# Performance work log

Hardware: AMD Instinct MI355X
Metric: run time of the kernel (lower is better)

## Reference

```python
import jax, jax.numpy as jnp
import numpy as np

B, DIM, HEADS, WS, H, W = 8, 192, 6, 8, 128, 128
HD = DIM // HEADS


def _make_coords(h, w, ws):
    # matches torch buffers: channel 0 = x (width axis), channel 1 = y (height axis)
    ref_w = jnp.linspace(-1.0, 1.0, w)
    ref_h = jnp.linspace(-1.0, 1.0, h)
    img_ref = jnp.stack(jnp.meshgrid(ref_w, ref_h, indexing='ij'), 0).transpose(0, 2, 1)  # (2,h,w)
    wh, ww = h // ws, w // ws
    win_ref = img_ref.reshape(2, wh, ws, ww, ws).mean(axis=(2, 4)).reshape(2, wh, 1, ww, 1)
    bch = jnp.arange(ws) * 2.0 / (h - 1); bch = bch - bch.mean()
    bcw = jnp.arange(ws) * 2.0 / (w - 1); bcw = bcw - bcw.mean()
    ech = jnp.tile(bch, wh)                      # (wh*ws,)
    ecw = jnp.tile(bcw, ww)                      # (ww*ws,)
    offs = jnp.stack(jnp.meshgrid(ecw, ech, indexing='ij'), 0).transpose(0, 2, 1)  # (2, wh*ws, ww*ws)
    offs = offs.reshape(2, wh, ws, ww, ws)
    return win_ref + offs, offs


def _rel_index(ws):
    ch, cw = np.meshgrid(np.arange(ws), np.arange(ws), indexing='ij')
    cf = np.stack([ch.ravel(), cw.ravel()])           # (2, ws*ws)
    rel = cf[:, :, None] - cf[:, None, :]             # (2, n, n)
    return jnp.asarray((rel[0] + ws - 1) * (2 * ws - 1) + (rel[1] + ws - 1))


def _grid_sample(img, grid):
    # F.grid_sample: bilinear, padding_mode='zeros', align_corners=True
    # img (N,C,H,W), grid (N,Ho,Wo,2) with [..,0]=x, [..,1]=y in [-1,1]
    n, c, h, w = img.shape
    gx = (grid[..., 0] + 1.0) * 0.5 * (w - 1)
    gy = (grid[..., 1] + 1.0) * 0.5 * (h - 1)
    x0 = jnp.floor(gx); y0 = jnp.floor(gy)
    wx1 = gx - x0; wy1 = gy - y0

    def gather(ix, iy, wgt):
        valid = (ix >= 0) & (ix <= w - 1) & (iy >= 0) & (iy <= h - 1)
        ixc = jnp.clip(ix, 0, w - 1).astype(jnp.int32)
        iyc = jnp.clip(iy, 0, h - 1).astype(jnp.int32)
        vals = jax.vmap(lambda im, yy, xx: im[:, yy, xx])(img, iyc, ixc)  # (N,C,Ho,Wo)
        return vals * (wgt * valid)[:, None]

    return (gather(x0, y0, (1 - wx1) * (1 - wy1)) + gather(x0 + 1, y0, wx1 * (1 - wy1))
            + gather(x0, y0 + 1, (1 - wx1) * wy1) + gather(x0 + 1, y0 + 1, wx1 * wy1))


def _forward(x, var, qkv_w, qkv_b, bias_w, bias_b, scale_w, scale_b, proj_w, proj_b, rel_table):
    b, c, h, w = x.shape
    wh, ww = h // WS, w // WS
    n_pred = b * HEADS
    base, offs = _make_coords(h, w, WS)

    topk = int(0.8 * h * w)
    var3 = var.reshape(b, c, h * w)
    _, idx = jax.lax.top_k(var3, topk)
    bi = jnp.arange(b)[:, None, None]; ci = jnp.arange(c)[None, :, None]
    mask = jnp.zeros((b, c, h * w), bool).at[bi, ci, idx].set(True)
    x_var = x * jnp.where(mask, 1.0, 0.6).reshape(b, c, h, w).astype(x.dtype)

    # sampling biases/scales: AvgPool(ws) -> LeakyReLU -> 1x1 conv
    pooled = jax.nn.leaky_relu(x_var.reshape(b, c, wh, WS, ww, WS).mean(axis=(3, 5)))
    biases = (jnp.einsum('bchw,oc->bohw', pooled, bias_w) + bias_b[None, :, None, None])
    biases = biases.reshape(n_pred, 2, wh, ww) / jnp.array([w // WS, h // WS], x.dtype)[None, :, None, None]
    scales = (jnp.einsum('bchw,oc->bohw', pooled, scale_w) + scale_b[None, :, None, None]).reshape(n_pred, 2, wh, ww)

    coords = base[None] + offs[None] * scales[:, :, :, None, :, None] + biases[:, :, :, None, :, None]
    grid = coords.transpose(0, 2, 3, 4, 5, 1).reshape(n_pred, h, w, 2)

    # qkv 1x1 conv, split into per-head maps
    qkv = jnp.einsum('bchw,oc->bohw', x, qkv_w) + qkv_b[None, :, None, None]
    qkv = qkv.reshape(b, 3, HEADS, HD, h, w).transpose(1, 0, 2, 3, 4, 5).reshape(3, n_pred, HD, h, w)
    q, k, v = qkv[0], qkv[1], qkv[2]

    ks = _grid_sample(k, grid)
    vs = _grid_sample(v, grid)

    def to_windows(t):  # (b*heads, hd, h, w) -> (b*wh*ww, heads, ws*ws, hd)
        return t.reshape(b, HEADS, HD, wh, WS, ww, WS).transpose(0, 3, 5, 1, 4, 6, 2).reshape(b * wh * ww, HEADS, WS * WS, HD)

    qw, kw, vw = to_windows(q), to_windows(ks), to_windows(vs)
    scores = jnp.einsum('wnid,wnjd->wnij', qw, kw) * (HD ** -0.5)
    rel_bias = rel_table[_rel_index(WS)].transpose(2, 0, 1)  # (heads, ws*ws, ws*ws)
    attn = jax.nn.softmax(scores + rel_bias[None], axis=-1)
    out = jnp.einsum('wnij,wnjd->wnid', attn, vw)
    out = out.reshape(b, wh, ww, HEADS, WS, WS, HD).transpose(0, 3, 6, 1, 4, 2, 5).reshape(b, c, h, w)
    return jnp.einsum('bchw,oc->bohw', out, proj_w) + proj_b[None, :, None, None]


def setup_inputs() -> dict:
    key = jax.random.key(0)
    ks = jax.random.split(key, 8)
    f = jnp.float32
    return {
        'x': jax.random.normal(ks[0], (B, DIM, H, W), f),
        'var': jax.random.uniform(ks[1], (B, DIM, H, W), f),
        'qkv_w': jax.random.normal(ks[2], (3 * DIM, DIM), f) * 0.05,
        'qkv_b': jnp.zeros((3 * DIM,), f),
        'bias_w': jax.random.normal(ks[3], (2 * HEADS, DIM), f) * 0.05,
        'bias_b': jnp.zeros((2 * HEADS,), f),
        'scale_w': jax.random.normal(ks[4], (2 * HEADS, DIM), f) * 0.05,
        'scale_b': jnp.zeros((2 * HEADS,), f),
        'proj_w': jax.random.normal(ks[5], (DIM, DIM), f) * 0.05,
        'proj_b': jnp.zeros((DIM,), f),
        'rel_table': jax.random.normal(ks[6], ((2 * WS - 1) ** 2, HEADS), f) * 0.02,
    }


def reference(x, var, qkv_w, qkv_b, bias_w, bias_b, scale_w, scale_b, proj_w, proj_b, rel_table):
    return _forward(x, var, qkv_w, qkv_b, bias_w, bias_b, scale_w, scale_b, proj_w, proj_b, rel_table)
```

## Files before the change

### kernel.cpp

```cpp
#include <hip/hip_runtime.h>
#include <hip/hip_bf16.h>
#include <math.h>

constexpr int BB = 8, CCH = 192, IH = 128, IW = 128;
constexpr int WSZ = 8;
constexpr int NWIN = 256;
constexpr int NH = 6, HDIM = 32;
constexpr int NPIX = IH * IW;
constexpr int TOPK = 13107;

typedef __attribute__((ext_vector_type(8))) short bf16x8;
typedef __attribute__((ext_vector_type(4))) float f32x4;
typedef __attribute__((ext_vector_type(4))) unsigned short u16x4;
typedef __attribute__((ext_vector_type(8))) unsigned short u16x8;

__device__ __forceinline__ unsigned short f2bf(float f) {
    __hip_bfloat16 h = __float2bfloat16(f);
    return __builtin_bit_cast(unsigned short, h);
}
__device__ __forceinline__ float bf2f(unsigned short u) {
    return __uint_as_float((unsigned)u << 16);
}
__device__ __forceinline__ unsigned monot(float f) {
    unsigned u = __float_as_uint(f);
    return (u & 0x80000000u) ? ~u : (u | 0x80000000u);
}

struct K1Smem {
    unsigned histP[2][2048];
    unsigned hist256[256];
    unsigned wtot[8];
    unsigned s_prefix, s_rem, s_cnt, s_thr, s_need;
    unsigned candKey[320], candIdx[320];
    unsigned cand_cnt, eq_cnt;
    unsigned eq_idx[64];
    float pooled_s[256];
};
struct K0Smem {
    unsigned short T[64][200];
};
constexpr size_t MEGA1_SMEM = sizeof(K0Smem) > sizeof(K1Smem) ? sizeof(K0Smem) : sizeof(K1Smem);

__global__ __launch_bounds__(512) void mega1(const float* __restrict__ x,
                                             const float* __restrict__ var,
                                             float* __restrict__ pooled,
                                             unsigned short* __restrict__ xt,
                                             const float* __restrict__ qkv_w,
                                             const float* __restrict__ proj_w,
                                             unsigned short* __restrict__ wbf,
                                             int fast) {
    __shared__ __align__(16) char smem[MEGA1_SMEM];
    int id = blockIdx.x;
    int tid = threadIdx.x;
    int wv = tid >> 6, lane = tid & 63;

    if (id < 72) {
        int i4 = id * 512 + tid;
        float4 v = (i4 < 27648) ? ((const float4*)qkv_w)[i4]
                                : ((const float4*)proj_w)[i4 - 27648];
        u16x4 pk = { f2bf(v.x), f2bf(v.y), f2bf(v.z), f2bf(v.w) };
        ((u16x4*)wbf)[i4] = pk;
        return;
    }
    id -= 72;

    int role, sub;
    if (fast) {
        int g = id / 7, r = id % 7;
        if (r < 3) { role = 0; sub = 3 * g + r; }
        else       { role = 1; sub = 4 * g + (r - 3); }
    } else {
        role = 0; sub = id;
    }

    if (role == 1) {
        K0Smem& S0 = *(K0Smem*)smem;
        int b = sub >> 8, px0 = (sub & 255) * 64;
        int px = tid & 63, cg = tid >> 6;
#pragma unroll
        for (int j8 = 0; j8 < 3; ++j8) {
            u16x8 pk;
#pragma unroll
            for (int j = 0; j < 8; ++j)
                pk[j] = f2bf(x[(size_t)(b * CCH + cg * 24 + j8 * 8 + j) * NPIX + px0 + px]);
            *(u16x8*)&S0.T[px][cg * 24 + j8 * 8] = pk;
        }
        __syncthreads();
#pragma unroll
        for (int i = 0; i < 3; ++i) {
            int u = tid + 512 * i;
            int p2 = u / 24, cb = u % 24;
            *(u16x8*)&xt[((size_t)(b * NPIX) + px0 + p2) * CCH + cb * 8] = *(const u16x8*)&S0.T[p2][cb * 8];
        }
        return;
    }

    K1Smem& S = *(K1Smem*)smem;
    int row = sub;
    const float4* vrow4 = (const float4*)(var + (size_t)row * NPIX);
    const float4* xrow4 = (const float4*)(x + (size_t)row * NPIX);
    const float* xrow = x + (size_t)row * NPIX;
    constexpr int CAP = 320;

    for (int i = tid; i < 2 * 2048; i += 512) ((unsigned*)S.histP)[i] = 0;
    if (tid < 256) S.pooled_s[tid] = 0.f;
    if (tid == 0) { S.cand_cnt = 0; S.eq_cnt = 0; }
    __syncthreads();

    int hc = lane & 1;
#pragma unroll
    for (int j = 0; j < 8; ++j) {
        float4 v4 = vrow4[tid + 512 * j];
        float vv[4] = {v4.x, v4.y, v4.z, v4.w};
#pragma unroll
        for (int c = 0; c < 4; ++c) {
            unsigned bk = monot(vv[c]) >> 20;
            atomicAdd(&S.histP[hc][bk >> 1], 1u << ((bk & 1) << 4));
        }
    }
    __syncthreads();

    {
        unsigned h8[8]; unsigned tsum = 0;
#pragma unroll
        for (int w = 0; w < 4; ++w) {
            unsigned w0 = S.histP[0][tid * 4 + w];
            unsigned w1 = S.histP[1][tid * 4 + w];
            h8[2 * w]     = (w0 & 0xFFFFu) + (w1 & 0xFFFFu);
            h8[2 * w + 1] = (w0 >> 16) + (w1 >> 16);
            tsum += h8[2 * w] + h8[2 * w + 1];
        }
        unsigned s = tsum;
#pragma unroll
        for (int off = 1; off < 64; off <<= 1) {
            unsigned t = __shfl(s, lane + off);
            if (lane + off < 64) s += t;
        }
        if (lane == 0) S.wtot[wv] = s;
        __syncthreads();
        unsigned crossTot = 0;
        for (int w = wv + 1; w < 8; ++w) crossTot += S.wtot[w];
        unsigned above = crossTot + (s - tsum);
        if (above < TOPK && above + tsum >= TOPK) {
            unsigned cum = above;
            for (int i = 7; i >= 0; --i) {
                if (cum < TOPK && cum + h8[i] >= TOPK) {
                    S.s_prefix = (unsigned)(tid * 8 + i);
                    S.s_rem = TOPK - cum;
                    S.s_cnt = h8[i];
                }
                cum += h8[i];
            }
        }
    }
    __syncthreads();

    unsigned prefix = S.s_prefix, rem2 = S.s_rem, cnt = S.s_cnt;
    int prefbits = 12;

    while (cnt > CAP && prefbits < 32) {
        int nb = (32 - prefbits >= 8) ? 8 : (32 - prefbits);
        int nbuck = 1 << nb;
        __syncthreads();
        for (int i = tid; i < nbuck; i += 512) S.hist256[i] = 0;
        __syncthreads();
        int shift = 32 - prefbits - nb;
#pragma unroll
        for (int j = 0; j < 8; ++j) {
            float4 v4 = vrow4[tid + 512 * j];
            float vv[4] = {v4.x, v4.y, v4.z, v4.w};
#pragma unroll
            for (int c = 0; c < 4; ++c) {
                unsigned mm = monot(vv[c]);
                if ((mm >> (nb + shift)) == prefix)
                    atomicAdd(&S.hist256[(mm >> shift) & (nbuck - 1)], 1u);
            }
        }
        __syncthreads();
        if (wv == 0) {
            int bpl = nbuck > 64 ? nbuck / 64 : 1;
            int nlanes = nbuck / bpl;
            unsigned hh[4] = {0, 0, 0, 0};
            unsigned lsum = 0;
#pragma unroll
            for (int i = 0; i < 4; ++i) {
                if (i < bpl && lane < nlanes) hh[i] = S.hist256[lane * bpl + i];
                lsum += hh[i];
            }
            unsigned s = lsum;
#pragma unroll
            for (int off = 1; off < 64; off <<= 1) {
                unsigned t = __shfl(s, lane + off);
                if (lane + off < 64) s += t;
            }
            unsigned above = s - lsum;
            if (lane < nlanes && above < rem2 && above + lsum >= rem2) {
                unsigned cum = above;
                for (int i = bpl - 1; i >= 0; --i) {
                    if (cum < rem2 && cum + hh[i] >= rem2) {
                        S.s_prefix = (prefix << nb) | (unsigned)(lane * bpl + i);
                        S.s_rem = rem2 - cum;
                        S.s_cnt = hh[i];
                    }
                    cum += hh[i];
                }
            }
        }
        __syncthreads();
        prefix = S.s_prefix; rem2 = S.s_rem; cnt = S.s_cnt;
        prefbits += nb;
    }

    int pshift = 32 - prefbits;

#pragma unroll
    for (int j = 0; j < 8; ++j) {
        float4 v4 = vrow4[tid + 512 * j];
        float4 x4 = xrow4[tid + 512 * j];
        float vv[4] = {v4.x, v4.y, v4.z, v4.w};
        float xv[4] = {x4.x, x4.y, x4.z, x4.w};
        float part = 0.f;
#pragma unroll
        for (int c = 0; c < 4; ++c) {
            unsigned mm = monot(vv[c]);
            unsigned g = (pshift == 0) ? mm : (mm >> pshift);
            float mult = (g > prefix) ? 1.0f : 0.6f;
            if (g == prefix) {
                unsigned pos = atomicAdd(&S.cand_cnt, 1u);
                if (pos < CAP) {
                    S.candKey[pos] = mm;
                    S.candIdx[pos] = (unsigned)(4 * tid + 2048 * j + c);
                }
            }
            part += xv[c] * mult;
        }
        part += __shfl_xor(part, 1);
        part += __shfl_xor(part, 32);
        if ((lane & 1) == 0 && lane < 32)
            atomicAdd(&S.pooled_s[(2 * j + (tid >> 8)) * 16 + ((tid >> 1) & 15)], part);
    }
    __syncthreads();

    int cc = (int)min(S.cand_cnt, (unsigned)CAP);
    for (int ci = tid; ci < cc; ci += 512) {
        unsigned my = S.candKey[ci];
        unsigned kgt = 0, keq = 0;
        for (int e = 0; e < cc; ++e) {
            unsigned o = S.candKey[e];
            kgt += (o > my);
            keq += (o == my);
        }
        if (kgt < rem2 && kgt + keq >= rem2) {
            S.s_thr = my;
            S.s_need = rem2 - kgt;
        }
    }
    __syncthreads();
    unsigned thr = S.s_thr, need_eq = S.s_need;
    for (int ci = tid; ci < cc; ci += 512)
        if (S.candKey[ci] == thr) {
            unsigned pos = atomicAdd(&S.eq_cnt, 1u);
            if (pos < 64) S.eq_idx[pos] = S.candIdx[ci];
        }
    __syncthreads();
    int ecnt = (int)min(S.eq_cnt, 64u);
    if (tid == 0) {
        for (int a = 1; a < ecnt; ++a) {
            unsigned key = S.eq_idx[a]; int q = a - 1;
            while (q >= 0 && S.eq_idx[q] > key) { S.eq_idx[q + 1] = S.eq_idx[q]; --q; }
            S.eq_idx[q + 1] = key;
        }
    }
    __syncthreads();

    for (int ci = tid; ci < cc; ci += 512) {
        unsigned key = S.candKey[ci], idx = S.candIdx[ci];
        bool inset;
        if (key > thr) inset = true;
        else if (key < thr) inset = false;
        else {
            unsigned rank = 0;
            for (int e = 0; e < ecnt; ++e) rank += (S.eq_idx[e] < idx);
            inset = (rank < need_eq);
        }
        if (inset) {
            int y = (int)(idx >> 7), xx = (int)(idx & 127);
            atomicAdd(&S.pooled_s[(y >> 3) * 16 + (xx >> 3)], 0.4f * xrow[idx]);
        }
    }
    __syncthreads();

    if (tid < 256) {
        float s = S.pooled_s[tid] * (1.0f / 64.0f);
        float pv = s > 0.f ? s : 0.01f * s;
        pooled[(size_t)row * NWIN + tid] = pv;
    }
}

template <bool FAST>
__global__ __launch_bounds__(256) void mega2(const float* __restrict__ x,
                                             const unsigned short* __restrict__ xt,
                                             const unsigned short* __restrict__ wq,
                                             const float* __restrict__ qkv_b,
                                             unsigned short* __restrict__ qb,
                                             unsigned short* __restrict__ kb,
                                             unsigned short* __restrict__ vb,
                                             const float* __restrict__ pooled,
                                             const float* __restrict__ bias_w,
                                             const float* __restrict__ bias_b,
                                             const float* __restrict__ scale_w,
                                             const float* __restrict__ scale_b,
                                             float* __restrict__ sb) {
    constexpr int BN = 128, KC = 64, KCP = 72;
    __shared__ unsigned short Ws[CCH][KCP];
    __shared__ unsigned short Xt[BN][KCP];
    int id = blockIdx.x;
    int tid = threadIdx.x;
    int g = id / 7, r = id % 7;

    if (r == 0) {
        float* pcol = (float*)&Ws[0][0];
        float* res = pcol + 4 * CCH;
        int wv = tid >> 6, lane = tid & 63;
        int blk = g * 4 + wv;
        int b = blk >> 8, w = blk & 255;
        for (int c = lane; c < CCH; c += 64) pcol[wv * CCH + c] = pooled[(size_t)(b * CCH + c) * NWIN + w];
        __syncthreads();
        if (lane < 24) {
            bool isScale = lane >= 12;
            int o = isScale ? lane - 12 : lane;
            const float* Wt = isScale ? scale_w : bias_w;
            float acc = 0.f;
            for (int c = 0; c < CCH; ++c) acc += Wt[o * CCH + c] * pcol[wv * CCH + c];
            acc += (isScale ? scale_b[o] : bias_b[o]);
            if (!isScale) acc *= (1.0f / 16.0f);
            res[wv * 24 + lane] = acc;
        }
        __syncthreads();
        if (lane < NH) {
            int p = b * NH + lane;
            float4 v;
            v.x = res[wv * 24 + 12 + 2 * lane];
            v.y = res[wv * 24 + 12 + 2 * lane + 1];
            v.z = res[wv * 24 + 2 * lane];
            v.w = res[wv * 24 + 2 * lane + 1];
            ((float4*)sb)[(size_t)p * NWIN + w] = v;
        }
        return;
    }

    int k3id = 6 * g + (r - 1);
    int px0 = (k3id & 127) * BN;
    int t = (k3id >> 7) % 3;
    int b = k3id / 384;
    int o0 = t * CCH;
    int wv = tid >> 6, lane = tid & 63, lr = lane & 15, lg = lane >> 4;

    f32x4 acc[3][8];
#pragma unroll
    for (int i = 0; i < 3; ++i)
#pragma unroll
        for (int j = 0; j < 8; ++j) acc[i][j] = (f32x4){0.f, 0.f, 0.f, 0.f};

    int spx = tid & 127, skg = tid >> 7;

    for (int k0 = 0; k0 < CCH; k0 += KC) {
#pragma unroll
        for (int i = 0; i < 6; ++i) {
            int u = tid + 256 * i;
            int o = u >> 3, kb8 = u & 7;
            *(u16x8*)&Ws[o][kb8 * 8] = *(const u16x8*)&wq[(size_t)(o0 + o) * CCH + k0 + kb8 * 8];
        }
        if (FAST) {
#pragma unroll
            for (int i = 0; i < 4; ++i) {
                int u = tid + 256 * i;
                int px = u >> 3, kb8 = u & 7;
                *(u16x8*)&Xt[px][kb8 * 8] =
                    *(const u16x8*)&xt[((size_t)(b * NPIX) + px0 + px) * CCH + k0 + kb8 * 8];
            }
        } else {
            const float* xcol = &x[(size_t)(b * CCH + k0 + skg * 32) * NPIX + px0 + spx];
#pragma unroll
            for (int j8 = 0; j8 < 4; ++j8) {
                u16x8 pk;
#pragma unroll
                for (int j = 0; j < 8; ++j) pk[j] = f2bf(xcol[(size_t)(j8 * 8 + j) * NPIX]);
                *(u16x8*)&Xt[spx][skg * 32 + j8 * 8] = pk;
            }
        }
        __syncthreads();
#pragma unroll
        for (int kk = 0; kk < KC; kk += 32) {
            bf16x8 af[3], bfr[8];
#pragma unroll
            for (int i = 0; i < 3; ++i)
                af[i] = *(const bf16x8*)&Ws[wv * 48 + i * 16 + lr][kk + lg * 8];
#pragma unroll
            for (int j = 0; j < 8; ++j)
                bfr[j] = *(const bf16x8*)&Xt[j * 16 + lr][kk + lg * 8];
#pragma unroll
            for (int i = 0; i < 3; ++i)
#pragma unroll
                for (int j = 0; j < 8; ++j)
                    acc[i][j] = __builtin_amdgcn_mfma_f32_16x16x32_bf16(af[i], bfr[j], acc[i][j], 0, 0, 0);
        }
        __syncthreads();
    }

#pragma unroll
    for (int i = 0; i < 3; ++i) {
        int och = wv * 48 + i * 16 + lg * 4;
        float b0 = qkv_b[o0 + och], b1 = qkv_b[o0 + och + 1];
        float b2 = qkv_b[o0 + och + 2], b3 = qkv_b[o0 + och + 3];
#pragma unroll
        for (int j = 0; j < 8; ++j) {
            int px = px0 + lr + j * 16;
            u16x4 pk = { f2bf(acc[i][j][0] + b0), f2bf(acc[i][j][1] + b1),
                         f2bf(acc[i][j][2] + b2), f2bf(acc[i][j][3] + b3) };
            if (t == 0) {
                *(u16x4*)&qb[((size_t)b * NPIX + px) * CCH + och] = pk;
            } else {
                int head = och >> 5, d = och & 31;
                unsigned short* dst = (t == 1) ? kb : vb;
                *(u16x4*)&dst[(((size_t)(b * NH + head)) * NPIX + px) * HDIM + d] = pk;
            }
        }
    }
}

__global__ __launch_bounds__(256) void k4_attn(unsigned short* __restrict__ qatt,
                                               const unsigned short* __restrict__ kb,
                                               const unsigned short* __restrict__ vb,
                                               const float* __restrict__ sb,
                                               const float* __restrict__ rel_table) {
    int tid = threadIdx.x;
    int wv = tid >> 6, lane = tid & 63, lr = lane & 15, lg = lane >> 4;
    int head = blockIdx.y, b = blockIdx.z;
    int win = blockIdx.x * 4 + wv;
    int wy = win >> 4, wx = win & 15;
    int p = b * NH + head;

    __shared__ float rel_s[225];
    __shared__ unsigned short Vl[4][64][33];
    __shared__ unsigned short Pl[4][64][68];

    if (tid < 225) rel_s[tid] = rel_table[tid * NH + head];

    bf16x8 qf[4];
#pragma unroll
    for (int tq = 0; tq < 4; ++tq) {
        int q = tq * 16 + lr;
        int pix = (wy * 8 + (q >> 3)) * IW + wx * 8 + (q & 7);
        qf[tq] = *(const bf16x8*)&qatt[((size_t)b * NPIX + pix) * CCH + head * HDIM + lg * 8];
    }

    float4 sbv = ((const float4*)sb)[(size_t)p * NWIN + win];
    bf16x8 kf[4];
#pragma unroll
    for (int mi = 0; mi < 4; ++mi) {
        int px = mi * 16 + lr;
        int dy = px >> 3, dx = px & 7;
        int yg = wy * 8 + dy, xg = wx * 8 + dx;
        float gx = -1.0f + xg * (2.0f / 127.0f) + ((float)dx - 3.5f) * (2.0f / 127.0f) * sbv.x + sbv.z;
        float gy = -1.0f + yg * (2.0f / 127.0f) + ((float)dy - 3.5f) * (2.0f / 127.0f) * sbv.y + sbv.w;
        float fx = (gx + 1.0f) * 0.5f * 127.0f;
        float fy = (gy + 1.0f) * 0.5f * 127.0f;
        float x0f = floorf(fx), y0f = floorf(fy);
        float wx1 = fx - x0f, wy1 = fy - y0f;
        int ix0 = (int)x0f, iy0 = (int)y0f;
        int ix1 = ix0 + 1, iy1 = iy0 + 1;
        float w00 = (1.0f - wx1) * (1.0f - wy1);
        float w10 = wx1 * (1.0f - wy1);
        float w01 = (1.0f - wx1) * wy1;
        float w11 = wx1 * wy1;
        bool vX0 = (ix0 >= 0) && (ix0 < IW), vX1 = (ix1 >= 0) && (ix1 < IW);
        bool vY0 = (iy0 >= 0) && (iy0 < IH), vY1 = (iy1 >= 0) && (iy1 < IH);
        if (!(vX0 && vY0)) w00 = 0.f;
        if (!(vX1 && vY0)) w10 = 0.f;
        if (!(vX0 && vY1)) w01 = 0.f;
        if (!(vX1 && vY1)) w11 = 0.f;
        int cx0 = min(max(ix0, 0), IW - 1), cx1 = min(max(ix1, 0), IW - 1);
        int cy0 = min(max(iy0, 0), IH - 1), cy1 = min(max(iy1, 0), IH - 1);
        size_t r00 = ((size_t)p * NPIX + cy0 * IW + cx0) * HDIM + lg * 8;
        size_t r10 = ((size_t)p * NPIX + cy0 * IW + cx1) * HDIM + lg * 8;
        size_t r01 = ((size_t)p * NPIX + cy1 * IW + cx0) * HDIM + lg * 8;
        size_t r11 = ((size_t)p * NPIX + cy1 * IW + cx1) * HDIM + lg * 8;
        u16x8 k00 = *(const u16x8*)&kb[r00], k10 = *(const u16x8*)&kb[r10];
        u16x8 k01 = *(const u16x8*)&kb[r01], k11 = *(const u16x8*)&kb[r11];
        u16x8 v00 = *(const u16x8*)&vb[r00], v10 = *(const u16x8*)&vb[r10];
        u16x8 v01 = *(const u16x8*)&vb[r01], v11 = *(const u16x8*)&vb[r11];
#pragma unroll
        for (int c = 0; c < 8; ++c) {
            float kvv = w00 * bf2f(k00[c]) + w10 * bf2f(k10[c]) +
                        w01 * bf2f(k01[c]) + w11 * bf2f(k11[c]);
            float vvv = w00 * bf2f(v00[c]) + w10 * bf2f(v10[c]) +
                        w01 * bf2f(v01[c]) + w11 * bf2f(v11[c]);
            kf[mi][c] = (short)f2bf(kvv);
            Vl[wv][px][lg * 8 + c] = f2bf(vvv);
        }
    }

    f32x4 acc[4][4];
#pragma unroll
    for (int tk = 0; tk < 4; ++tk)
#pragma unroll
        for (int tq = 0; tq < 4; ++tq) acc[tk][tq] = (f32x4){0.f, 0.f, 0.f, 0.f};
#pragma unroll
    for (int tk = 0; tk < 4; ++tk)
#pragma unroll
        for (int tq = 0; tq < 4; ++tq)
            acc[tk][tq] = __builtin_amdgcn_mfma_f32_16x16x32_bf16(kf[tk], qf[tq], acc[tk][tq], 0, 0, 0);

    __syncthreads();

    const float scale = 0.17677669529663688f;
    int qh[4], qwv[4];
#pragma unroll
    for (int tq = 0; tq < 4; ++tq) { int q = tq * 16 + lr; qh[tq] = q >> 3; qwv[tq] = q & 7; }
    float mx[4] = {-1e30f, -1e30f, -1e30f, -1e30f};
#pragma unroll
    for (int tk = 0; tk < 4; ++tk)
#pragma unroll
        for (int r = 0; r < 4; ++r) {
            int key = tk * 16 + lg * 4 + r;
            int kh = key >> 3, kw = key & 7;
#pragma unroll
            for (int tq = 0; tq < 4; ++tq) {
                float v = acc[tk][tq][r] * scale + rel_s[(qh[tq] - kh + 7) * 15 + (qwv[tq] - kw + 7)];
                acc[tk][tq][r] = v;
                mx[tq] = fmaxf(mx[tq], v);
            }
        }
#pragma unroll
    for (int tq = 0; tq < 4; ++tq) {
        mx[tq] = fmaxf(mx[tq], __shfl_xor(mx[tq], 16));
        mx[tq] = fmaxf(mx[tq], __shfl_xor(mx[tq], 32));
    }
    float sm[4] = {0.f, 0.f, 0.f, 0.f};
#pragma unroll
    for (int tk = 0; tk < 4; ++tk)
#pragma unroll
        for (int tq = 0; tq < 4; ++tq)
#pragma unroll
            for (int r = 0; r < 4; ++r) {
                float e = __expf(acc[tk][tq][r] - mx[tq]);
                acc[tk][tq][r] = e;
                sm[tq] += e;
            }
    float inv[4];
#pragma unroll
    for (int tq = 0; tq < 4; ++tq) {
        float s = sm[tq];
        s += __shfl_xor(s, 16);
        s += __shfl_xor(s, 32);
        inv[tq] = 1.0f / s;
    }
#pragma unroll
    for (int tq = 0; tq < 4; ++tq)
#pragma unroll
        for (int tk = 0; tk < 4; ++tk) {
            u16x4 pk = { f2bf(acc[tk][tq][0] * inv[tq]), f2bf(acc[tk][tq][1] * inv[tq]),
                         f2bf(acc[tk][tq][2] * inv[tq]), f2bf(acc[tk][tq][3] * inv[tq]) };
            *(u16x4*)&Pl[wv][tq * 16 + lr][tk * 16 + lg * 4] = pk;
        }

    __syncthreads();

    f32x4 o[4][2];
#pragma unroll
    for (int mq = 0; mq < 4; ++mq)
#pragma unroll
        for (int nd = 0; nd < 2; ++nd) o[mq][nd] = (f32x4){0.f, 0.f, 0.f, 0.f};
#pragma unroll
    for (int ks = 0; ks < 2; ++ks) {
        bf16x8 Af[4];
#pragma unroll
        for (int mq = 0; mq < 4; ++mq) {
            u16x4 lo = *(const u16x4*)&Pl[wv][mq * 16 + lr][ks * 32 + lg * 8];
            u16x4 hi = *(const u16x4*)&Pl[wv][mq * 16 + lr][ks * 32 + lg * 8 + 4];
#pragma unroll
            for (int c = 0; c < 4; ++c) { Af[mq][c] = (short)lo[c]; Af[mq][c + 4] = (short)hi[c]; }
        }
        bf16x8 Bf[2];
#pragma unroll
        for (int nd = 0; nd < 2; ++nd)
#pragma unroll
            for (int j = 0; j < 8; ++j)
                Bf[nd][j] = (short)Vl[wv][ks * 32 + lg * 8 + j][nd * 16 + lr];
#pragma unroll
        for (int mq = 0; mq < 4; ++mq)
#pragma unroll
            for (int nd = 0; nd < 2; ++nd)
                o[mq][nd] = __builtin_amdgcn_mfma_f32_16x16x32_bf16(Af[mq], Bf[nd], o[mq][nd], 0, 0, 0);
    }

#pragma unroll
    for (int mq = 0; mq < 4; ++mq)
#pragma unroll
        for (int nd = 0; nd < 2; ++nd)
#pragma unroll
            for (int r = 0; r < 4; ++r) {
                int q = mq * 16 + lg * 4 + r;
                int pix = (wy * 8 + (q >> 3)) * IW + wx * 8 + (q & 7);
                qatt[((size_t)b * NPIX + pix) * CCH + head * HDIM + nd * 16 + lr] = f2bf(o[mq][nd][r]);
            }
}

__global__ __launch_bounds__(256) void k5_mfma(const unsigned short* __restrict__ att,
                                               const unsigned short* __restrict__ wp,
                                               const float* __restrict__ proj_b,
                                               float* __restrict__ out) {
    constexpr int BN = 128, KC = 64, KCP = 72;
    __shared__ unsigned short Ws[CCH][KCP];
    __shared__ unsigned short Xt[BN][KCP];
    int px0 = blockIdx.x * BN;
    int b = blockIdx.y;
    int tid = threadIdx.x;
    int wv = tid >> 6, lane = tid & 63, lr = lane & 15, lg = lane >> 4;

    f32x4 acc[3][8];
#pragma unroll
    for (int i = 0; i < 3; ++i)
#pragma unroll
        for (int j = 0; j < 8; ++j) acc[i][j] = (f32x4){0.f, 0.f, 0.f, 0.f};

    int spx = tid & 127, skg = tid >> 7;

    for (int k0 = 0; k0 < CCH; k0 += KC) {
#pragma unroll
        for (int i = 0; i < 6; ++i) {
            int u = tid + 256 * i;
            int o = u >> 3, kb8 = u & 7;
            *(u16x8*)&Ws[o][kb8 * 8] = *(const u16x8*)&wp[(size_t)o * CCH + k0 + kb8 * 8];
        }
        {
            const unsigned short* arow = &att[((size_t)b * NPIX + px0 + spx) * CCH + k0 + skg * 32];
#pragma unroll
            for (int j8 = 0; j8 < 4; ++j8)
                *(u16x8*)&Xt[spx][skg * 32 + j8 * 8] = *(const u16x8*)&arow[j8 * 8];
        }
        __syncthreads();
#pragma unroll
        for (int kk = 0; kk < KC; kk += 32) {
            bf16x8 af[3], bfr[8];
#pragma unroll
            for (int i = 0; i < 3; ++i)
                af[i] = *(const bf16x8*)&Ws[wv * 48 + i * 16 + lr][kk + lg * 8];
#pragma unroll
            for (int j = 0; j < 8; ++j)
                bfr[j] = *(const bf16x8*)&Xt[j * 16 + lr][kk + lg * 8];
#pragma unroll
            for (int i = 0; i < 3; ++i)
#pragma unroll
                for (int j = 0; j < 8; ++j)
                    acc[i][j] = __builtin_amdgcn_mfma_f32_16x16x32_bf16(af[i], bfr[j], acc[i][j], 0, 0, 0);
        }
        __syncthreads();
    }

#pragma unroll
    for (int i = 0; i < 3; ++i) {
        int och = wv * 48 + i * 16 + lg * 4;
#pragma unroll
        for (int r = 0; r < 4; ++r) {
            float bias = proj_b[och + r];
            size_t base = (size_t)(b * CCH + och + r) * NPIX + px0 + lr;
#pragma unroll
            for (int j = 0; j < 8; ++j)
                out[base + j * 16] = acc[i][j][r] + bias;
        }
    }
}

extern "C" void kernel_launch(void* const* d_in, const int* in_sizes, int n_in,
                              void* d_out, int out_size, void* d_ws, size_t ws_size,
                              hipStream_t stream) {
    const float* x = (const float*)d_in[0];
    const float* var = (const float*)d_in[1];
    const float* qkv_w = (const float*)d_in[2];
    const float* qkv_b = (const float*)d_in[3];
    const float* bias_w = (const float*)d_in[4];
    const float* bias_b = (const float*)d_in[5];
    const float* scale_w = (const float*)d_in[6];
    const float* scale_b = (const float*)d_in[7];
    const float* proj_w = (const float*)d_in[8];
    const float* proj_b = (const float*)d_in[9];
    const float* rel_table = (const float*)d_in[10];
    float* out = (float*)d_out;

    char* ws = (char*)d_ws;
    float* pooled = (float*)ws;
    float* sb = (float*)(ws + 1572864ull);
    const size_t elemQ = (size_t)BB * CCH * NPIX;
    unsigned short* q = (unsigned short*)(ws + 1769472ull);
    unsigned short* k = q + elemQ;
    unsigned short* v = k + elemQ;
    unsigned short* wbf = v + elemQ;
    unsigned short* wq_bf = wbf;
    unsigned short* wp_bf = wbf + 110592;
    unsigned short* xt = wbf + 147456;

    size_t need_base = 1769472ull + 3ull * elemQ * 2 + 294912ull;
    size_t need_fast = need_base + elemQ * 2;
    if (ws_size < need_base) return;
    bool fast = ws_size >= need_fast;

    mega1<<<dim3(72 + (fast ? 3584 : 1536)), dim3(512), 0, stream>>>(
        x, var, pooled, xt, qkv_w, proj_w, wbf, fast ? 1 : 0);

    if (fast) {
        mega2<true><<<dim3(3584), dim3(256), 0, stream>>>(x, xt, wq_bf, qkv_b, q, k, v,
                                                          pooled, bias_w, bias_b, scale_w, scale_b, sb);
    } else {
        mega2<false><<<dim3(3584), dim3(256), 0, stream>>>(x, xt, wq_bf, qkv_b, q, k, v,
                                                           pooled, bias_w, bias_b, scale_w, scale_b, sb);
    }

    k4_attn<<<dim3(NWIN / 4, NH, BB), dim3(256), 0, stream>>>(q, k, v, sb, rel_table);
    k5_mfma<<<dim3(NPIX / 128, BB), dim3(256), 0, stream>>>(q, wp_bf, proj_b, out);
}
```

Before: 267.1 us.

## Pass softmax probabilities to PV MFMA via lane shuffles instead of LDS

In the windowed attention kernel, the probability matrix is no longer staged through a shared-memory buffer (Pl). Each MFMA A-operand for the P·V product is built from the QK accumulators with cross-lane shuffles, which removes one LDS round trip and one block-wide barrier. The barrier moves to before the QK MFMAs, and s_setprio hints are placed around the MFMA sequences. In exchange it issues many ds_bpermute shuffles (two per element plus a select), which may cost as much as the LDS traffic they replace.

```diff
diff --git a/kernel.cpp b/kernel.cpp
--- a/kernel.cpp
+++ b/kernel.cpp
@@ -443,7 +443,6 @@
 
     __shared__ float rel_s[225];
     __shared__ unsigned short Vl[4][64][33];
-    __shared__ unsigned short Pl[4][64][68];
 
     if (tid < 225) rel_s[tid] = rel_table[tid * NH + head];
 
@@ -501,18 +500,20 @@
         }
     }
 
+    __syncthreads();
+
     f32x4 acc[4][4];
 #pragma unroll
     for (int tk = 0; tk < 4; ++tk)
 #pragma unroll
         for (int tq = 0; tq < 4; ++tq) acc[tk][tq] = (f32x4){0.f, 0.f, 0.f, 0.f};
+    __builtin_amdgcn_s_setprio(1);
 #pragma unroll
     for (int tk = 0; tk < 4; ++tk)
 #pragma unroll
         for (int tq = 0; tq < 4; ++tq)
             acc[tk][tq] = __builtin_amdgcn_mfma_f32_16x16x32_bf16(kf[tk], qf[tq], acc[tk][tq], 0, 0, 0);
-
-    __syncthreads();
+    __builtin_amdgcn_s_setprio(0);
 
     const float scale = 0.17677669529663688f;
     int qh[4], qwv[4];
@@ -548,25 +549,20 @@
                 acc[tk][tq][r] = e;
                 sm[tq] += e;
             }
-    float inv[4];
 #pragma unroll
     for (int tq = 0; tq < 4; ++tq) {
         float s = sm[tq];
         s += __shfl_xor(s, 16);
         s += __shfl_xor(s, 32);
-        inv[tq] = 1.0f / s;
-    }
-#pragma unroll
-    for (int tq = 0; tq < 4; ++tq)
-#pragma unroll
-        for (int tk = 0; tk < 4; ++tk) {
-            u16x4 pk = { f2bf(acc[tk][tq][0] * inv[tq]), f2bf(acc[tk][tq][1] * inv[tq]),
-                         f2bf(acc[tk][tq][2] * inv[tq]), f2bf(acc[tk][tq][3] * inv[tq]) };
-            *(u16x4*)&Pl[wv][tq * 16 + lr][tk * 16 + lg * 4] = pk;
-        }
-
-    __syncthreads();
-
+        float inv = 1.0f / s;
+#pragma unroll
+        for (int tk = 0; tk < 4; ++tk)
+#pragma unroll
+            for (int r = 0; r < 4; ++r) acc[tk][tq][r] *= inv;
+    }
+
+    int s0 = lr + 16 * (2 * (lg & 1));
+    int tksel = (lg >> 1) & 1;
     f32x4 o[4][2];
 #pragma unroll
     for (int mq = 0; mq < 4; ++mq)
@@ -574,14 +570,6 @@
         for (int nd = 0; nd < 2; ++nd) o[mq][nd] = (f32x4){0.f, 0.f, 0.f, 0.f};
 #pragma unroll
     for (int ks = 0; ks < 2; ++ks) {
-        bf16x8 Af[4];
-#pragma unroll
-        for (int mq = 0; mq < 4; ++mq) {
-            u16x4 lo = *(const u16x4*)&Pl[wv][mq * 16 + lr][ks * 32 + lg * 8];
-            u16x4 hi = *(const u16x4*)&Pl[wv][mq * 16 + lr][ks * 32 + lg * 8 + 4];
-#pragma unroll
-            for (int c = 0; c < 4; ++c) { Af[mq][c] = (short)lo[c]; Af[mq][c + 4] = (short)hi[c]; }
-        }
         bf16x8 Bf[2];
 #pragma unroll
         for (int nd = 0; nd < 2; ++nd)
@@ -589,10 +577,21 @@
             for (int j = 0; j < 8; ++j)
                 Bf[nd][j] = (short)Vl[wv][ks * 32 + lg * 8 + j][nd * 16 + lr];
 #pragma unroll
-        for (int mq = 0; mq < 4; ++mq)
+        for (int mq = 0; mq < 4; ++mq) {
+            bf16x8 Af;
+#pragma unroll
+            for (int j = 0; j < 8; ++j) {
+                int sl = s0 + 16 * (j >> 2);
+                float f0 = __shfl(acc[2 * ks + 0][mq][j & 3], sl);
+                float f1 = __shfl(acc[2 * ks + 1][mq][j & 3], sl);
+                Af[j] = (short)f2bf(tksel ? f1 : f0);
+            }
+            __builtin_amdgcn_s_setprio(1);
 #pragma unroll
             for (int nd = 0; nd < 2; ++nd)
-                o[mq][nd] = __builtin_amdgcn_mfma_f32_16x16x32_bf16(Af[mq], Bf[nd], o[mq][nd], 0, 0, 0);
+                o[mq][nd] = __builtin_amdgcn_mfma_f32_16x16x32_bf16(Af, Bf[nd], o[mq][nd], 0, 0, 0);
+            __builtin_amdgcn_s_setprio(0);
+        }
     }
 
 #pragma unroll
```

Result: slower. 275.8 us (+3.2%).
